# Kernel tuning notes

Measured on AMD Instinct MI355X. Metric: run time of the kernel, lower is better.

## Reference

```python
import jax, jax.numpy as jnp
import numpy as np

B = 8192
L = 2  # number of clipped photonic layers


def _pauli_z_matrix():
    # Z expectation per wire for each of the 16 basis states; wire 0 = MSB.
    k = np.arange(16)
    Z = np.stack([1 - 2 * ((k >> 3) & 1),
                  1 - 2 * ((k >> 2) & 1),
                  1 - 2 * ((k >> 1) & 1),
                  1 - 2 * (k & 1)], axis=1).astype(np.float32)
    return jnp.asarray(Z)  # (16, 4)


def setup_inputs() -> dict:
    key = jax.random.key(0)
    ks = jax.random.split(key, 14)
    x = jax.random.normal(ks[0], (B, 1, 28, 28), dtype=jnp.float32)
    # input photonic layer (no clip)
    w_in = 0.5 * jax.random.normal(ks[1], (2, 2), dtype=jnp.float32)
    b_in = 0.1 * jax.random.normal(ks[2], (2,), dtype=jnp.float32)
    scale_in = 1.0 + 0.1 * jax.random.normal(ks[3], (2,), dtype=jnp.float32)
    shift_in = 0.05 * jax.random.normal(ks[4], (2,), dtype=jnp.float32)
    # L clipped photonic layers (clip applied at construction in torch)
    Wc = jnp.clip(0.5 * jax.random.normal(ks[5], (L, 2, 2), dtype=jnp.float32), -5.0, 5.0)
    bc = jnp.clip(0.1 * jax.random.normal(ks[6], (L, 2), dtype=jnp.float32), -5.0, 5.0)
    scalec = 1.0 + 0.1 * jax.random.normal(ks[7], (L, 2), dtype=jnp.float32)
    shiftc = 0.05 * jax.random.normal(ks[8], (L, 2), dtype=jnp.float32)
    # final linear of classical branch: Linear(2, 1)
    w_out = 0.5 * jax.random.normal(ks[9], (1, 2), dtype=jnp.float32)
    b_out = 0.1 * jax.random.normal(ks[10], (1,), dtype=jnp.float32)
    # fixed random 16x16 unitary standing in for tq.RandomLayer(n_ops=8, 4 wires)
    rng = np.random.default_rng(0)
    A = rng.normal(size=(16, 16)) + 1j * rng.normal(size=(16, 16))
    Q, _ = np.linalg.qr(A)
    U_re = jnp.asarray(Q.real.astype(np.float32))
    U_im = jnp.asarray(Q.imag.astype(np.float32))
    # classifier Linear(785, 1)  (original declares 786 but combined feat is 785)
    w_cls = 0.03 * jax.random.normal(ks[11], (1, 785), dtype=jnp.float32)
    b_cls = 0.1 * jax.random.normal(ks[12], (1,), dtype=jnp.float32)
    return {"x": x, "w_in": w_in, "b_in": b_in, "scale_in": scale_in,
            "shift_in": shift_in, "Wc": Wc, "bc": bc, "scalec": scalec,
            "shiftc": shiftc, "w_out": w_out, "b_out": b_out,
            "U_re": U_re, "U_im": U_im, "w_cls": w_cls, "b_cls": b_cls}


def reference(x, w_in, b_in, scale_in, shift_in, Wc, bc, scalec, shiftc,
              w_out, b_out, U_re, U_im, w_cls, b_cls):
    bsz = x.shape[0]
    # ---- classical branch: mean/std features through photonic-style MLP ----
    mean = jnp.mean(x, axis=(1, 2, 3))[:, None]
    std = jnp.std(x, axis=(1, 2, 3), ddof=1)[:, None]  # torch unbiased std
    h = jnp.concatenate([mean, std], axis=1)  # (B, 2)
    h = jnp.tanh(h @ w_in.T + b_in) * scale_in + shift_in
    for i in range(Wc.shape[0]):
        h = jnp.tanh(h @ Wc[i].T + bc[i]) * scalec[i] + shiftc[i]
    cls_out = h @ w_out.T + b_out  # (B, 1)
    # ---- quantum branch: all 196 2x2 patches batched in one pass ----
    img = x.reshape(bsz, 28, 28)
    # (B,14,2,14,2) -> (B,14,14,2,2) -> (B,196,4) with patch pixel order
    # [x[r,c], x[r,c+1], x[r+1,c], x[r+1,c+1]] matching the torch loop.
    p = img.reshape(bsz, 14, 2, 14, 2).transpose(0, 1, 3, 2, 4).reshape(bsz, 196, 4)
    half = 0.5 * p
    a = jnp.stack([jnp.cos(half), jnp.sin(half)], axis=-1)  # (B,196,4,2) RY|0> amps
    # product state over 4 qubits -> (B,196,16)
    psi = jnp.einsum('bpi,bpj,bpk,bpl->bpijkl',
                     a[:, :, 0], a[:, :, 1], a[:, :, 2], a[:, :, 3]
                     ).reshape(bsz, 196, 16)
    re = psi @ U_re.T
    im = psi @ U_im.T
    probs = re * re + im * im  # (B,196,16)
    Z = _pauli_z_matrix()
    qfeat = (probs @ Z).reshape(bsz, 196 * 4)  # (B, 784)
    # ---- fuse + classify ----
    combined = jnp.concatenate([cls_out, qfeat], axis=1)  # (B, 785)
    logits = combined @ w_cls.T + b_cls
    return jax.nn.sigmoid(logits)
```

## Files before the change

### kernel.cpp

```cpp
#include <hip/hip_runtime.h>
#include <math.h>


#define NPATCH 196
#define NIMG   8192
#define NTOTAL (NIMG * NPATCH)

__global__ __launch_bounds__(256) void patch_kernel(
    const float* __restrict__ x,
    const float* __restrict__ U_re,
    const float* __restrict__ U_im,
    const float* __restrict__ w_cls,
    float* __restrict__ accS,
    float* __restrict__ accSS,
    float* __restrict__ accQ)
{
    const int g    = blockIdx.x * 256 + threadIdx.x;
    const int img  = g / NPATCH;
    const int p    = g - img * NPATCH;
    const int r    = p / 14;
    const int c    = p - r * 14;
    const int lane = threadIdx.x & 63;

    const float* xp = x + (size_t)img * 784;
    const float2 top = *(const float2*)(xp + (2 * r) * 28 + 2 * c);
    const float2 bot = *(const float2*)(xp + (2 * r + 1) * 28 + 2 * c);
    const float x0 = top.x, x1 = top.y, x2 = bot.x, x3 = bot.y;

    float sum   = x0 + x1 + x2 + x3;
    float sumsq = x0 * x0 + x1 * x1 + x2 * x2 + x3 * x3;

    const float c0 = __cosf(0.5f * x0), s0 = __sinf(0.5f * x0);
    const float c1 = __cosf(0.5f * x1), s1 = __sinf(0.5f * x1);
    const float c2 = __cosf(0.5f * x2), s2 = __sinf(0.5f * x2);
    const float c3 = __cosf(0.5f * x3), s3 = __sinf(0.5f * x3);

    float p01[4] = { c0 * c1, c0 * s1, s0 * c1, s0 * s1 };
    float p23[4] = { c2 * c3, c2 * s3, s2 * c3, s2 * s3 };
    float psi[16];
    #pragma unroll
    for (int h = 0; h < 4; ++h)
        #pragma unroll
        for (int l = 0; l < 4; ++l)
            psi[h * 4 + l] = p01[h] * p23[l];

    const float wq0 = w_cls[1 + p * 4 + 0];
    const float wq1 = w_cls[1 + p * 4 + 1];
    const float wq2 = w_cls[1 + p * 4 + 2];
    const float wq3 = w_cls[1 + p * 4 + 3];
    float hi[4] = { wq0 + wq1, wq0 - wq1, -wq0 + wq1, -wq0 - wq1 };
    float lo[4] = { wq2 + wq3, wq2 - wq3, -wq2 + wq3, -wq2 - wq3 };

    float qsum = 0.f;
    #pragma unroll
    for (int k = 0; k < 16; ++k) {
        const float* ur = U_re + k * 16;
        const float* ui = U_im + k * 16;
        float re = 0.f, im = 0.f;
        #pragma unroll
        for (int m = 0; m < 16; ++m) {
            re = fmaf(ur[m], psi[m], re);
            im = fmaf(ui[m], psi[m], im);
        }
        const float prob = re * re + im * im;
        qsum = fmaf(prob, hi[k >> 2] + lo[k & 3], qsum);
    }

    const int imgF = __builtin_amdgcn_readfirstlane(img);
    const bool first = (img == imgF);
    float aS = first ? sum   : 0.f;  float bS = sum   - aS;
    float aV = first ? sumsq : 0.f;  float bV = sumsq - aV;
    float aQ = first ? qsum  : 0.f;  float bQ = qsum  - aQ;

    #pragma unroll
    for (int off = 1; off < 64; off <<= 1) {
        aS += __shfl_xor(aS, off, 64);  bS += __shfl_xor(bS, off, 64);
        aV += __shfl_xor(aV, off, 64);  bV += __shfl_xor(bV, off, 64);
        aQ += __shfl_xor(aQ, off, 64);  bQ += __shfl_xor(bQ, off, 64);
    }

    if (lane == 0) {
        atomicAdd(accS  + imgF, aS);
        atomicAdd(accSS + imgF, aV);
        atomicAdd(accQ  + imgF, aQ);
    }
    if (lane == 63 && img != imgF) {
        atomicAdd(accS  + img, bS);
        atomicAdd(accSS + img, bV);
        atomicAdd(accQ  + img, bQ);
    }
}

__global__ __launch_bounds__(256) void final_kernel(
    const float* __restrict__ accS,
    const float* __restrict__ accSS,
    const float* __restrict__ accQ,
    const float* __restrict__ w_in,
    const float* __restrict__ b_in,
    const float* __restrict__ scale_in,
    const float* __restrict__ shift_in,
    const float* __restrict__ Wc,
    const float* __restrict__ bc,
    const float* __restrict__ scalec,
    const float* __restrict__ shiftc,
    const float* __restrict__ w_out,
    const float* __restrict__ b_out,
    const float* __restrict__ w_cls,
    const float* __restrict__ b_cls,
    float* __restrict__ out)
{
    const int i = blockIdx.x * 256 + threadIdx.x;
    const float S  = accS[i];
    const float SS = accSS[i];
    const float QS = accQ[i];

    const float mean = S * (1.f / 784.f);
    float var = (SS - S * S * (1.f / 784.f)) * (1.f / 783.f);
    var = fmaxf(var, 0.f);
    const float stdv = sqrtf(var);

    float h0 = mean, h1 = stdv;
    {
        const float t0 = tanhf(h0 * w_in[0] + h1 * w_in[1] + b_in[0]);
        const float t1 = tanhf(h0 * w_in[2] + h1 * w_in[3] + b_in[1]);
        h0 = t0 * scale_in[0] + shift_in[0];
        h1 = t1 * scale_in[1] + shift_in[1];
    }
    #pragma unroll
    for (int l = 0; l < 2; ++l) {
        const float t0 = tanhf(h0 * Wc[l * 4 + 0] + h1 * Wc[l * 4 + 1] + bc[l * 2 + 0]);
        const float t1 = tanhf(h0 * Wc[l * 4 + 2] + h1 * Wc[l * 4 + 3] + bc[l * 2 + 1]);
        h0 = t0 * scalec[l * 2 + 0] + shiftc[l * 2 + 0];
        h1 = t1 * scalec[l * 2 + 1] + shiftc[l * 2 + 1];
    }
    const float cls   = h0 * w_out[0] + h1 * w_out[1] + b_out[0];
    const float logit = b_cls[0] + w_cls[0] * cls + QS;
    out[i] = 1.f / (1.f + __expf(-logit));
}

extern "C" void kernel_launch(void* const* d_in, const int* in_sizes, int n_in,
                              void* d_out, int out_size, void* d_ws, size_t ws_size,
                              hipStream_t stream) {
    const float* x        = (const float*)d_in[0];
    const float* w_in     = (const float*)d_in[1];
    const float* b_in     = (const float*)d_in[2];
    const float* scale_in = (const float*)d_in[3];
    const float* shift_in = (const float*)d_in[4];
    const float* Wc       = (const float*)d_in[5];
    const float* bc       = (const float*)d_in[6];
    const float* scalec   = (const float*)d_in[7];
    const float* shiftc   = (const float*)d_in[8];
    const float* w_out    = (const float*)d_in[9];
    const float* b_out    = (const float*)d_in[10];
    const float* U_re     = (const float*)d_in[11];
    const float* U_im     = (const float*)d_in[12];
    const float* w_cls    = (const float*)d_in[13];
    const float* b_cls    = (const float*)d_in[14];
    float* out = (float*)d_out;

    float* accS  = (float*)d_ws;
    float* accSS = accS + NIMG;
    float* accQ  = accSS + NIMG;

    hipMemsetAsync(d_ws, 0, 3 * NIMG * sizeof(float), stream);

    patch_kernel<<<NTOTAL / 256, 256, 0, stream>>>(x, U_re, U_im, w_cls,
                                                   accS, accSS, accQ);
    final_kernel<<<NIMG / 256, 256, 0, stream>>>(accS, accSS, accQ,
                                                 w_in, b_in, scale_in, shift_in,
                                                 Wc, bc, scalec, shiftc,
                                                 w_out, b_out, w_cls, b_cls, out);
}
```

Measured before the change: 127.4 us.

## Compute patch unitary and Pauli-Z projection with bf16 MFMA via LDS staging

Each thread's 16-amplitude product state is packed to bf16 into shared memory. Each wave then runs 16x16x32 bf16 MFMAs against the real and imaginary parts of U to get amplitudes, squares them into probabilities, and runs a second MFMA against the Pauli-Z matrix. This replaces the per-thread 512-FMA scalar matvec with matrix-core work. In exchange it adds bf16 rounding of the state, the unitary and the probabilities, several LDS round trips with block barriers, and zero-padding of the K dimension to 32.

New measurement: 133.1 us. 4.5% more time.

```diff
diff --git a/kernel.cpp b/kernel.cpp
--- a/kernel.cpp
+++ b/kernel.cpp
@@ -1,10 +1,25 @@
 #include <hip/hip_runtime.h>
+#include <hip/hip_bf16.h>
 #include <math.h>
 
 
 #define NPATCH 196
 #define NIMG   8192
 #define NTOTAL (NIMG * NPATCH)
+#define ROWB   80
+
+typedef __bf16 bf16x8 __attribute__((ext_vector_type(8)));
+typedef float  f32x4  __attribute__((ext_vector_type(4)));
+
+union Frag { bf16x8 v; uint4 u; unsigned us[4]; };
+
+static __device__ inline unsigned short bfbits(float f) {
+    __hip_bfloat16 h = __float2bfloat16(f);
+    unsigned short s; __builtin_memcpy(&s, &h, 2); return s;
+}
+static __device__ inline unsigned packbf(float lo, float hi) {
+    return (unsigned)bfbits(lo) | ((unsigned)bfbits(hi) << 16);
+}
 
 __global__ __launch_bounds__(256) void patch_kernel(
     const float* __restrict__ x,
@@ -15,58 +30,132 @@
     float* __restrict__ accSS,
     float* __restrict__ accQ)
 {
-    const int g    = blockIdx.x * 256 + threadIdx.x;
-    const int img  = g / NPATCH;
-    const int p    = g - img * NPATCH;
-    const int r    = p / 14;
-    const int c    = p - r * 14;
-    const int lane = threadIdx.x & 63;
+    __shared__ __align__(16) unsigned char lds[256 * ROWB];
+    __shared__ float qlds[256];
+
+    const int tid  = threadIdx.x;
+    const int lane = tid & 63;
+    const int wv   = tid >> 6;
+    const int n16  = lane & 15;
+    const int q    = lane >> 4;
+
+    Frag bre, bim, bz;
+    bre.u = make_uint4(0u, 0u, 0u, 0u);
+    bim.u = make_uint4(0u, 0u, 0u, 0u);
+    if (q < 2) {
+        const float* pr = U_re + n16 * 16 + q * 8;
+        const float* pi = U_im + n16 * 16 + q * 8;
+        bre.us[0] = packbf(pr[0], pr[1]); bre.us[1] = packbf(pr[2], pr[3]);
+        bre.us[2] = packbf(pr[4], pr[5]); bre.us[3] = packbf(pr[6], pr[7]);
+        bim.us[0] = packbf(pi[0], pi[1]); bim.us[1] = packbf(pi[2], pi[3]);
+        bim.us[2] = packbf(pi[4], pi[5]); bim.us[3] = packbf(pi[6], pi[7]);
+    }
+    #pragma unroll
+    for (int jj = 0; jj < 4; ++jj) {
+        float v0 = 0.f, v1 = 0.f;
+        if (q < 2 && n16 < 4) {
+            const int k0 = q * 8 + 2 * jj;
+            v0 = ((k0 >> (3 - n16)) & 1) ? -1.f : 1.f;
+            v1 = (((k0 + 1) >> (3 - n16)) & 1) ? -1.f : 1.f;
+        }
+        bz.us[jj] = packbf(v0, v1);
+    }
+
+    const int gp  = blockIdx.x * 256 + tid;
+    const int img = gp / NPATCH;
+    const int p   = gp - img * NPATCH;
+    const int rr  = p / 14;
+    const int cc  = p - rr * 14;
 
     const float* xp = x + (size_t)img * 784;
-    const float2 top = *(const float2*)(xp + (2 * r) * 28 + 2 * c);
-    const float2 bot = *(const float2*)(xp + (2 * r + 1) * 28 + 2 * c);
+    const float2 top = *(const float2*)(xp + (2 * rr) * 28 + 2 * cc);
+    const float2 bot = *(const float2*)(xp + (2 * rr + 1) * 28 + 2 * cc);
     const float x0 = top.x, x1 = top.y, x2 = bot.x, x3 = bot.y;
 
-    float sum   = x0 + x1 + x2 + x3;
-    float sumsq = x0 * x0 + x1 * x1 + x2 * x2 + x3 * x3;
-
-    const float c0 = __cosf(0.5f * x0), s0 = __sinf(0.5f * x0);
-    const float c1 = __cosf(0.5f * x1), s1 = __sinf(0.5f * x1);
-    const float c2 = __cosf(0.5f * x2), s2 = __sinf(0.5f * x2);
-    const float c3 = __cosf(0.5f * x3), s3 = __sinf(0.5f * x3);
-
-    float p01[4] = { c0 * c1, c0 * s1, s0 * c1, s0 * s1 };
-    float p23[4] = { c2 * c3, c2 * s3, s2 * c3, s2 * s3 };
-    float psi[16];
-    #pragma unroll
-    for (int h = 0; h < 4; ++h)
-        #pragma unroll
-        for (int l = 0; l < 4; ++l)
-            psi[h * 4 + l] = p01[h] * p23[l];
-
-    const float wq0 = w_cls[1 + p * 4 + 0];
-    const float wq1 = w_cls[1 + p * 4 + 1];
-    const float wq2 = w_cls[1 + p * 4 + 2];
-    const float wq3 = w_cls[1 + p * 4 + 3];
-    float hi[4] = { wq0 + wq1, wq0 - wq1, -wq0 + wq1, -wq0 - wq1 };
-    float lo[4] = { wq2 + wq3, wq2 - wq3, -wq2 + wq3, -wq2 - wq3 };
-
-    float qsum = 0.f;
-    #pragma unroll
-    for (int k = 0; k < 16; ++k) {
-        const float* ur = U_re + k * 16;
-        const float* ui = U_im + k * 16;
-        float re = 0.f, im = 0.f;
-        #pragma unroll
-        for (int m = 0; m < 16; ++m) {
-            re = fmaf(ur[m], psi[m], re);
-            im = fmaf(ui[m], psi[m], im);
-        }
-        const float prob = re * re + im * im;
-        qsum = fmaf(prob, hi[k >> 2] + lo[k & 3], qsum);
-    }
-
-    const int imgF = __builtin_amdgcn_readfirstlane(img);
+    const float sum   = x0 + x1 + x2 + x3;
+    const float sumsq = x0 * x0 + x1 * x1 + x2 * x2 + x3 * x3;
+
+    float s0, c0, s1, c1, s2, c2, s3, c3;
+    __sincosf(0.5f * x0, &s0, &c0);
+    __sincosf(0.5f * x1, &s1, &c1);
+    __sincosf(0.5f * x2, &s2, &c2);
+    __sincosf(0.5f * x3, &s3, &c3);
+
+    const float a01[4] = { c0 * c1, c0 * s1, s0 * c1, s0 * s1 };
+    const float a23[4] = { c2 * c3, c2 * s3, s2 * c3, s2 * s3 };
+
+    unsigned* row = (unsigned*)(lds + tid * ROWB);
+    uint4 lo, hi;
+    lo.x = packbf(a01[0] * a23[0], a01[0] * a23[1]);
+    lo.y = packbf(a01[0] * a23[2], a01[0] * a23[3]);
+    lo.z = packbf(a01[1] * a23[0], a01[1] * a23[1]);
+    lo.w = packbf(a01[1] * a23[2], a01[1] * a23[3]);
+    hi.x = packbf(a01[2] * a23[0], a01[2] * a23[1]);
+    hi.y = packbf(a01[2] * a23[2], a01[2] * a23[3]);
+    hi.z = packbf(a01[3] * a23[0], a01[3] * a23[1]);
+    hi.w = packbf(a01[3] * a23[2], a01[3] * a23[3]);
+    *(uint4*)(row)      = lo;
+    *(uint4*)(row + 4)  = hi;
+    *(uint4*)(row + 8)  = make_uint4(0u, 0u, 0u, 0u);
+    *(uint4*)(row + 12) = make_uint4(0u, 0u, 0u, 0u);
+    __syncthreads();
+
+    const unsigned char* wb = lds + wv * 64 * ROWB;
+    f32x4 prob[4];
+    #pragma unroll
+    for (int t = 0; t < 4; ++t) {
+        Frag a;
+        a.u = *(const uint4*)(wb + (t * 16 + n16) * ROWB + q * 16);
+        f32x4 cr = {0.f, 0.f, 0.f, 0.f}, ci = {0.f, 0.f, 0.f, 0.f};
+        cr = __builtin_amdgcn_mfma_f32_16x16x32_bf16(a.v, bre.v, cr, 0, 0, 0);
+        ci = __builtin_amdgcn_mfma_f32_16x16x32_bf16(a.v, bim.v, ci, 0, 0, 0);
+        #pragma unroll
+        for (int j = 0; j < 4; ++j)
+            prob[t][j] = cr[j] * cr[j] + ci[j] * ci[j];
+    }
+    __syncthreads();
+
+    #pragma unroll
+    for (int t = 0; t < 4; ++t)
+        #pragma unroll
+        for (int j = 0; j < 4; ++j)
+            *(unsigned short*)(lds + (wv * 64 + t * 16 + q * 4 + j) * ROWB + n16 * 2)
+                = bfbits(prob[t][j]);
+    __syncthreads();
+
+    #pragma unroll
+    for (int t = 0; t < 4; ++t) {
+        Frag ap;
+        ap.u = *(const uint4*)(wb + (t * 16 + n16) * ROWB + q * 16);
+        f32x4 y = {0.f, 0.f, 0.f, 0.f};
+        y = __builtin_amdgcn_mfma_f32_16x16x32_bf16(ap.v, bz.v, y, 0, 0, 0);
+        float v[4];
+        #pragma unroll
+        for (int j = 0; j < 4; ++j) {
+            float wq = 0.f;
+            if (n16 < 4) {
+                const int gg  = blockIdx.x * 256 + wv * 64 + t * 16 + q * 4 + j;
+                const int im2 = gg / NPATCH;
+                const int pp  = gg - im2 * NPATCH;
+                wq = w_cls[1 + 4 * pp + n16];
+            }
+            v[j] = y[j] * wq;
+        }
+        #pragma unroll
+        for (int j = 0; j < 4; ++j) {
+            v[j] += __shfl_xor(v[j], 1, 64);
+            v[j] += __shfl_xor(v[j], 2, 64);
+        }
+        if (n16 == 0) {
+            *(float4*)(qlds + wv * 64 + t * 16 + q * 4)
+                = make_float4(v[0], v[1], v[2], v[3]);
+        }
+    }
+    __syncthreads();
+
+    const float qsum = qlds[tid];
+
+    const int imgF  = __builtin_amdgcn_readfirstlane(img);
     const bool first = (img == imgF);
     float aS = first ? sum   : 0.f;  float bS = sum   - aS;
     float aV = first ? sumsq : 0.f;  float bV = sumsq - aV;
@@ -95,18 +184,12 @@
     const float* __restrict__ accS,
     const float* __restrict__ accSS,
     const float* __restrict__ accQ,
-    const float* __restrict__ w_in,
-    const float* __restrict__ b_in,
-    const float* __restrict__ scale_in,
-    const float* __restrict__ shift_in,
-    const float* __restrict__ Wc,
-    const float* __restrict__ bc,
-    const float* __restrict__ scalec,
-    const float* __restrict__ shiftc,
-    const float* __restrict__ w_out,
-    const float* __restrict__ b_out,
-    const float* __restrict__ w_cls,
-    const float* __restrict__ b_cls,
+    const float* __restrict__ w_in, const float* __restrict__ b_in,
+    const float* __restrict__ scale_in, const float* __restrict__ shift_in,
+    const float* __restrict__ Wc, const float* __restrict__ bc,
+    const float* __restrict__ scalec, const float* __restrict__ shiftc,
+    const float* __restrict__ w_out, const float* __restrict__ b_out,
+    const float* __restrict__ w_cls, const float* __restrict__ b_cls,
     float* __restrict__ out)
 {
     const int i = blockIdx.x * 256 + threadIdx.x;
```
